# Kernel tuning notes

Hardware: AMD Instinct MI355X
Metric: run time of the kernel (lower is better)

Reference implementation:

```python
import jax, jax.numpy as jnp
import numpy as np
import math

HEAD_DIM = 128
DEPTH = 12
LAMBDA_INIT = 0.8 - 0.6 * math.exp(-0.3 * DEPTH)
EPS = 1e-5


def setup_inputs() -> dict:
    key = jax.random.key(0)
    ks = jax.random.split(key, 7)
    B, S, H2, D = 2, 2048, 16, HEAD_DIM  # H2 = 2 * num_diff_heads
    q = jax.random.normal(ks[0], (B, S, H2, D), dtype=jnp.float32)
    k = jax.random.normal(ks[1], (B, S, H2, D), dtype=jnp.float32)
    v = jax.random.normal(ks[2], (B, S, H2, D), dtype=jnp.float32)
    lambda_q1 = 0.1 * jax.random.normal(ks[3], (D,), dtype=jnp.float32)
    lambda_k1 = 0.1 * jax.random.normal(ks[4], (D,), dtype=jnp.float32)
    lambda_q2 = 0.1 * jax.random.normal(ks[5], (D,), dtype=jnp.float32)
    lambda_k2 = 0.1 * jax.random.normal(ks[6], (D,), dtype=jnp.float32)
    return {"q": q, "k": k, "v": v, "lambda_q1": lambda_q1, "lambda_k1": lambda_k1,
            "lambda_q2": lambda_q2, "lambda_k2": lambda_k2}


def _attn(qh, kh, v12, scale, causal_bias):
    # qh,kh: [B,S,H,D]; v12: [B,S,H,2D] (concat of v1,v2 -> same softmax shared,
    # identical math to the two separate flash calls attnX1/attnX2 concatenated)
    scores = jnp.einsum('bshd,bthd->bhst', qh, kh) * scale + causal_bias
    p = jax.nn.softmax(scores, axis=-1)
    return jnp.einsum('bhst,bthd->bshd', p, v12)  # [B,S,H,2D]


def reference(q, k, v, lambda_q1, lambda_k1, lambda_q2, lambda_k2):
    B, S, H2, D = q.shape
    H = H2 // 2
    scale = 1.0 / math.sqrt(D)
    # split_heads: '(H two) D' -> pairs of adjacent heads
    def split(x):
        x = x.reshape(B, S, H, 2, D)
        return x[..., 0, :], x[..., 1, :]
    q1, q2 = split(q)
    k1, k2 = split(k)
    v1, v2 = split(v)
    v12 = jnp.concatenate([v1, v2], axis=-1)  # [B,S,H,2D]

    causal_bias = jnp.where(jnp.tril(jnp.ones((S, S), dtype=bool)), 0.0,
                            jnp.float32(-jnp.inf))  # [S,S]

    attn1 = _attn(q1, k1, v12, scale, causal_bias)  # = cat(attn11, attn12)
    attn2 = _attn(q2, k2, v12, scale, causal_bias)  # = cat(attn21, attn22)

    lambda_1 = jnp.exp(jnp.sum(lambda_q1 * lambda_k1))
    lambda_2 = jnp.exp(jnp.sum(lambda_q2 * lambda_k2))
    lambda_full = lambda_1 - lambda_2 + LAMBDA_INIT

    attn = attn1 - lambda_full * attn2  # [B,S,H,2D]
    # RMSNorm over last dim (2D), no affine
    attn = attn * jax.lax.rsqrt(jnp.mean(attn * attn, axis=-1, keepdims=True) + EPS)
    attn = attn * (1.0 - LAMBDA_INIT)
    # '... H (two D) -> ... (H two) D'
    return attn.reshape(B, S, H, 2, D).reshape(B, S, H2, D)
```

## Files before the change

kernel.cpp:

```cpp
#include <hip/hip_runtime.h>
#include <math.h>


#define S_LEN 2048
#define ROWSTR 2048
#define NEG_BIG (-3.0e38f)
#define QSCALE (1.44269504088896f * 0.0883883476483184f)
#define LAMBDA_INIT 0.783605766532f

typedef __attribute__((ext_vector_type(8))) short short8;
typedef __attribute__((ext_vector_type(4))) float f32x4;

__device__ __forceinline__ short f2bf(float f) {
    unsigned u = __builtin_bit_cast(unsigned, f);
    u += 0x7fffu + ((u >> 16) & 1u);
    return (short)(u >> 16);
}

__device__ __forceinline__ void async16(const short* g, short* l) {
    __builtin_amdgcn_global_load_lds(
        (const __attribute__((address_space(1))) unsigned int*)g,
        (__attribute__((address_space(3))) unsigned int*)l, 16, 0, 0);
}

__global__ __launch_bounds__(256)
void prep_kernel(const float* __restrict__ q, const float* __restrict__ k,
                 const float* __restrict__ v,
                 short* __restrict__ kws, short* __restrict__ vws,
                 short* __restrict__ qws) {
    const int tid = threadIdx.x;
    const int bh  = blockIdx.x >> 6;
    const int t   = blockIdx.x & 63;
    const int b   = bh >> 3;
    const int h   = bh & 7;

    {
        const int attn = tid >> 7;
        const int key  = (tid >> 2) & 31;
        const int tt   = tid & 3;
        const int s    = t * 32 + key;
        const float* src = k + (((size_t)(b * S_LEN + s) * 16) + 2 * h + attn) * 128 + tt * 32;
        const float* qsrc = q + (((size_t)(b * S_LEN + s) * 16) + 2 * h + attn) * 128 + tt * 32;
        short* kdst = kws + (((size_t)(bh * 64 + t)) << 13) + attn * 4096 + key * 128;
        const int rowtile = s >> 4;
        const int mi      = s & 15;
        short* qdst = qws + (((size_t)(bh * 2 + attn)) << 18) + (rowtile << 11) + (mi << 3);
        #pragma unroll
        for (int i = 0; i < 4; ++i) {
            const int c = tt * 4 + i;
            float4 a0 = *(const float4*)(src + i * 8);
            float4 a1 = *(const float4*)(src + i * 8 + 4);
            short8 sv;
            sv[0]=f2bf(a0.x); sv[1]=f2bf(a0.y); sv[2]=f2bf(a0.z); sv[3]=f2bf(a0.w);
            sv[4]=f2bf(a1.x); sv[5]=f2bf(a1.y); sv[6]=f2bf(a1.z); sv[7]=f2bf(a1.w);
            *(short8*)(kdst + ((c ^ (key & 7)) << 3)) = sv;
            a0 = *(const float4*)(qsrc + i * 8);
            a1 = *(const float4*)(qsrc + i * 8 + 4);
            sv[0]=f2bf(a0.x*QSCALE); sv[1]=f2bf(a0.y*QSCALE); sv[2]=f2bf(a0.z*QSCALE); sv[3]=f2bf(a0.w*QSCALE);
            sv[4]=f2bf(a1.x*QSCALE); sv[5]=f2bf(a1.y*QSCALE); sv[6]=f2bf(a1.z*QSCALE); sv[7]=f2bf(a1.w*QSCALE);
            *(short8*)(qdst + (c << 7)) = sv;
        }
    }

    {
        const int n = tid;
        const float* vsrc = v + (((size_t)(b * S_LEN + t * 32) * 16) + 2 * h + (n >> 7)) * 128 + (n & 127);
        short vv[32];
        #pragma unroll
        for (int key = 0; key < 32; ++key)
            vv[key] = f2bf(vsrc[(size_t)key * ROWSTR]);
        short* vdst = vws + (((size_t)(bh * 64 + t)) << 13) + n * 32;
        #pragma unroll
        for (int i = 0; i < 4; ++i)
            *(short8*)(vdst + i * 8) = *(short8*)&vv[i * 8];
    }
}

__global__ __launch_bounds__(256, 2)
void fda_kernel(const short* __restrict__ kws, const short* __restrict__ vws,
                const short* __restrict__ qws,
                const float* __restrict__ lq1, const float* __restrict__ lk1,
                const float* __restrict__ lq2, const float* __restrict__ lk2,
                float* __restrict__ out) {
    __shared__ short sK[2][2][32][128];
    __shared__ short sV[2][256][32];
    __shared__ short sP[2][64][40];
    __shared__ float sM[2][2];
    __shared__ float sL[2][64];
    __shared__ float sRed[2][2][32];

    const int tid  = threadIdx.x;
    const int w    = tid >> 6;
    const int lane = tid & 63;
    const int mi   = lane & 15;
    const int quad = lane >> 4;
    const int rg   = w & 1;
    const int u    = w >> 1;

    const int bid = blockIdx.x;
    const int bh  = bid & 15;
    const int g   = bid >> 4;
    const int qt  = (g < 16) ? (31 - g) : (g - 16);
    const int b   = bh >> 3;
    const int h   = bh & 7;
    const int qbase = qt * 64;
    const int nt  = 2 * qt + 2;

    float d1 = lq1[lane] * lk1[lane] + lq1[lane + 64] * lk1[lane + 64];
    float d2 = lq2[lane] * lk2[lane] + lq2[lane + 64] * lk2[lane + 64];
    #pragma unroll
    for (int off = 32; off; off >>= 1) {
        d1 += __shfl_xor(d1, off);
        d2 += __shfl_xor(d2, off);
    }
    const float lambda_full = expf(d1) - expf(d2) + LAMBDA_INIT;

    short8 qf[2][4];
    {
        const short* qb = qws + (((size_t)(bh * 2 + u)) << 18);
        #pragma unroll
        for (int m = 0; m < 2; ++m) {
            const int rowtile = qt * 4 + rg * 2 + m;
            #pragma unroll
            for (int db = 0; db < 4; ++db)
                qf[m][db] = *(const short8*)(qb + (rowtile << 11) + (((db << 2) + quad) << 7) + (mi << 3));
        }
    }

    float mold = -1e30f;
    float l[2][4] = {{0.f,0.f,0.f,0.f},{0.f,0.f,0.f,0.f}};
    f32x4 O[2][2][8];
    #pragma unroll
    for (int a = 0; a < 2; ++a)
        #pragma unroll
        for (int m = 0; m < 2; ++m)
            #pragma unroll
            for (int nb = 0; nb < 8; ++nb)
                O[a][m][nb] = (f32x4){0.f, 0.f, 0.f, 0.f};

    const short* ktile0 = kws + (((size_t)(bh * 64)) << 13);
    const short* vtile0 = vws + (((size_t)(bh * 64)) << 13);

    {
        short* dk = &sK[0][0][0][0];
        short* dv = &sV[0][0][0];
        #pragma unroll
        for (int i = 0; i < 4; ++i) {
            const int ch = (w * 4 + i) * 512;
            async16(ktile0 + ch + lane * 8, dk + ch);
            async16(vtile0 + ch + lane * 8, dv + ch);
        }
    }

    for (int t = 0; t < nt; ++t) {
        __syncthreads();
        const int buf = t & 1;
        const bool act = (t <= 2 * qt + rg);

        f32x4 S[2][2];
        if (act) {
            #pragma unroll
            for (int m = 0; m < 2; ++m)
                #pragma unroll
                for (int kh = 0; kh < 2; ++kh)
                    S[m][kh] = (f32x4){0.f, 0.f, 0.f, 0.f};
            const short* kb = &sK[buf][u][0][0];
            #pragma unroll
            for (int db = 0; db < 4; ++db) {
                #pragma unroll
                for (int kh = 0; kh < 2; ++kh) {
                    const short8 kf = *(const short8*)(kb + (kh * 16 + mi) * 128 +
                                       ((((db << 2) + quad) ^ (mi & 7)) << 3));
                    S[0][kh] = __builtin_amdgcn_mfma_f32_16x16x32_bf16(qf[0][db], kf, S[0][kh], 0, 0, 0);
                    S[1][kh] = __builtin_amdgcn_mfma_f32_16x16x32_bf16(qf[1][db], kf, S[1][kh], 0, 0, 0);
                }
            }
            if (t == 2 * qt + rg) {
                const int qr0 = qbase + rg * 32;
                #pragma unroll
                for (int m = 0; m < 2; ++m)
                    #pragma unroll
                    for (int kh = 0; kh < 2; ++kh)
                        #pragma unroll
                        for (int r = 0; r < 4; ++r)
                            if (t * 32 + kh * 16 + mi > qr0 + m * 16 + quad * 4 + r)
                                S[m][kh][r] = NEG_BIG;
            }
            float mx = -1e30f;
            #pragma unroll
            for (int m = 0; m < 2; ++m)
                #pragma unroll
                for (int kh = 0; kh < 2; ++kh)
                    mx = fmaxf(mx, fmaxf(fmaxf(S[m][kh][0], S[m][kh][1]),
                                         fmaxf(S[m][kh][2], S[m][kh][3])));
            #pragma unroll
            for (int off = 32; off; off >>= 1)
                mx = fmaxf(mx, __shfl_xor(mx, off));
            if (lane == 0) sM[rg][u] = mx;
        }
        __syncthreads();

        float alpha = 1.0f;
        if (act) {
            const float mnew = fmaxf(mold, fmaxf(sM[rg][0], sM[rg][1]));
            alpha = exp2f(mold - mnew);
            mold = mnew;
            #pragma unroll
            for (int m = 0; m < 2; ++m) {
                short* pp = &sP[u][rg * 32 + m * 16 + quad * 4][mi];
                #pragma unroll
                for (int r = 0; r < 4; ++r) {
                    const float pa = exp2f(S[m][0][r] - mnew);
                    const float pb = exp2f(S[m][1][r] - mnew);
                    l[m][r] = l[m][r] * alpha + (pa + pb);
                    pp[r * 40]      = f2bf(pa);
                    pp[r * 40 + 16] = f2bf(pb);
                }
            }
        }
        __syncthreads();

        if (t + 1 < nt) {
            const short* kt = ktile0 + (((size_t)(t + 1)) << 13);
            const short* vt = vtile0 + (((size_t)(t + 1)) << 13);
            short* dk = &sK[(t + 1) & 1][0][0][0];
            short* dv = &sV[(t + 1) & 1][0][0];
            #pragma unroll
            for (int i = 0; i < 4; ++i) {
                const int ch = (w * 4 + i) * 512;
                async16(kt + ch + lane * 8, dk + ch);
                async16(vt + ch + lane * 8, dv + ch);
            }
        }

        if (act) {
            if (alpha != 1.0f) {
                #pragma unroll
                for (int a = 0; a < 2; ++a)
                    #pragma unroll
                    for (int m = 0; m < 2; ++m)
                        #pragma unroll
                        for (int nb = 0; nb < 8; ++nb)
                            #pragma unroll
                            for (int r = 0; r < 4; ++r)
                                O[a][m][nb][r] *= alpha;
            }
            short8 pA[2][2];
            #pragma unroll
            for (int a = 0; a < 2; ++a)
                #pragma unroll
                for (int m = 0; m < 2; ++m)
                    pA[a][m] = *(const short8*)&sP[a][rg * 32 + m * 16 + mi][quad * 8];
            #pragma unroll
            for (int nb = 0; nb < 8; ++nb) {
                const short8 bv = *(const short8*)&sV[buf][u * 128 + nb * 16 + mi][quad * 8];
                O[0][0][nb] = __builtin_amdgcn_mfma_f32_16x16x32_bf16(pA[0][0], bv, O[0][0][nb], 0, 0, 0);
                O[0][1][nb] = __builtin_amdgcn_mfma_f32_16x16x32_bf16(pA[0][1], bv, O[0][1][nb], 0, 0, 0);
                O[1][0][nb] = __builtin_amdgcn_mfma_f32_16x16x32_bf16(pA[1][0], bv, O[1][0][nb], 0, 0, 0);
                O[1][1][nb] = __builtin_amdgcn_mfma_f32_16x16x32_bf16(pA[1][1], bv, O[1][1][nb], 0, 0, 0);
            }
        }
    }

    #pragma unroll
    for (int m = 0; m < 2; ++m)
        #pragma unroll
        for (int r = 0; r < 4; ++r) {
            float s = l[m][r];
            s += __shfl_xor(s, 1); s += __shfl_xor(s, 2);
            s += __shfl_xor(s, 4); s += __shfl_xor(s, 8);
            l[m][r] = s;
        }
    if (mi == 0) {
        #pragma unroll
        for (int m = 0; m < 2; ++m)
            #pragma unroll
            for (int r = 0; r < 4; ++r)
                sL[u][rg * 32 + m * 16 + quad * 4 + r] = l[m][r];
    }
    __syncthreads();

    float ss[2][4] = {{0.f,0.f,0.f,0.f},{0.f,0.f,0.f,0.f}};
    #pragma unroll
    for (int m = 0; m < 2; ++m)
        #pragma unroll
        for (int r = 0; r < 4; ++r) {
            const int row = rg * 32 + m * 16 + quad * 4 + r;
            const float il1 = 1.0f / sL[0][row];
            const float il2 = lambda_full / sL[1][row];
            #pragma unroll
            for (int nb = 0; nb < 8; ++nb) {
                const float c = O[0][m][nb][r] * il1 - O[1][m][nb][r] * il2;
                O[0][m][nb][r] = c;
                ss[m][r] += c * c;
            }
        }
    #pragma unroll
    for (int m = 0; m < 2; ++m)
        #pragma unroll
        for (int r = 0; r < 4; ++r) {
            float s = ss[m][r];
            s += __shfl_xor(s, 1); s += __shfl_xor(s, 2);
            s += __shfl_xor(s, 4); s += __shfl_xor(s, 8);
            ss[m][r] = s;
        }
    if (mi == 0) {
        #pragma unroll
        for (int m = 0; m < 2; ++m)
            #pragma unroll
            for (int r = 0; r < 4; ++r)
                sRed[rg][u][m * 16 + quad * 4 + r] = ss[m][r];
    }
    __syncthreads();

    #pragma unroll
    for (int m = 0; m < 2; ++m)
        #pragma unroll
        for (int r = 0; r < 4; ++r) {
            const int rl  = m * 16 + quad * 4 + r;
            const float tot = ss[m][r] + sRed[rg][u ^ 1][rl];
            const float scale = rsqrtf(tot * (1.0f / 256.0f) + 1e-5f) * (1.0f - LAMBDA_INIT);
            const int gr = qbase + rg * 32 + rl;
            float* ob = out + ((size_t)(b * S_LEN + gr)) * ROWSTR + h * 256 + u * 128 + mi;
            #pragma unroll
            for (int nb = 0; nb < 8; ++nb)
                ob[nb * 16] = O[0][m][nb][r] * scale;
        }
}

extern "C" void kernel_launch(void* const* d_in, const int* in_sizes, int n_in,
                              void* d_out, int out_size, void* d_ws, size_t ws_size,
                              hipStream_t stream) {
    (void)in_sizes; (void)n_in; (void)out_size; (void)ws_size;
    const float* q   = (const float*)d_in[0];
    const float* k   = (const float*)d_in[1];
    const float* v   = (const float*)d_in[2];
    const float* lq1 = (const float*)d_in[3];
    const float* lk1 = (const float*)d_in[4];
    const float* lq2 = (const float*)d_in[5];
    const float* lk2 = (const float*)d_in[6];
    float* out = (float*)d_out;

    short* kws = (short*)d_ws;
    short* vws = kws + (size_t)16 * 64 * 8192;
    short* qws = vws + (size_t)16 * 64 * 8192;

    prep_kernel<<<dim3(1024), dim3(256), 0, stream>>>(q, k, v, kws, vws, qws);
    fda_kernel<<<dim3(512), dim3(256), 0, stream>>>(kws, vws, qws,
                                                    lq1, lk1, lq2, lk2, out);
}
```

Baseline: 287.9 us.

## Warp-specialize attention into QK/softmax and PV warps with pipelined tiles

Rewrites the attention kernel to use 512-thread blocks in which four warps compute QK^T and softmax while four other warps compute the PV product one tile behind, passing probabilities and rescale factors through double-buffered shared memory. Each block now processes two query tiles (a long and a short one) to balance causal work, and the grid is halved. Q is converted to bf16 inside the attention kernel instead of in the prep pass, removing the Q workspace round trip. K/V workspace layouts change to remove swizzling, which may introduce LDS bank conflicts, and the larger block may lower occupancy.

Result: slower. 308.4 us (+7.1%).

```diff
diff --git a/kernel.cpp b/kernel.cpp
--- a/kernel.cpp
+++ b/kernel.cpp
@@ -24,10 +24,8 @@
 }
 
 __global__ __launch_bounds__(256)
-void prep_kernel(const float* __restrict__ q, const float* __restrict__ k,
-                 const float* __restrict__ v,
-                 short* __restrict__ kws, short* __restrict__ vws,
-                 short* __restrict__ qws) {
+void prep_kernel(const float* __restrict__ k, const float* __restrict__ v,
+                 short* __restrict__ kws, short* __restrict__ vws) {
     const int tid = threadIdx.x;
     const int bh  = blockIdx.x >> 6;
     const int t   = blockIdx.x & 63;
@@ -37,74 +35,64 @@
     {
         const int attn = tid >> 7;
         const int key  = (tid >> 2) & 31;
-        const int tt   = tid & 3;
-        const int s    = t * 32 + key;
-        const float* src = k + (((size_t)(b * S_LEN + s) * 16) + 2 * h + attn) * 128 + tt * 32;
-        const float* qsrc = q + (((size_t)(b * S_LEN + s) * 16) + 2 * h + attn) * 128 + tt * 32;
-        short* kdst = kws + (((size_t)(bh * 64 + t)) << 13) + attn * 4096 + key * 128;
-        const int rowtile = s >> 4;
-        const int mi      = s & 15;
-        short* qdst = qws + (((size_t)(bh * 2 + attn)) << 18) + (rowtile << 11) + (mi << 3);
+        const int dg   = tid & 3;
+        const float* src = k + ((size_t)(b * S_LEN + t * 32 + key) * 16 + 2 * h + attn) * 128 + dg * 32;
+        short* dstb = kws + ((size_t)(bh * 64 + t) << 13) + attn * 4096 + key * 8;
         #pragma unroll
         for (int i = 0; i < 4; ++i) {
-            const int c = tt * 4 + i;
-            float4 a0 = *(const float4*)(src + i * 8);
-            float4 a1 = *(const float4*)(src + i * 8 + 4);
+            const float4 a0 = *(const float4*)(src + i * 8);
+            const float4 a1 = *(const float4*)(src + i * 8 + 4);
             short8 sv;
             sv[0]=f2bf(a0.x); sv[1]=f2bf(a0.y); sv[2]=f2bf(a0.z); sv[3]=f2bf(a0.w);
             sv[4]=f2bf(a1.x); sv[5]=f2bf(a1.y); sv[6]=f2bf(a1.z); sv[7]=f2bf(a1.w);
-            *(short8*)(kdst + ((c ^ (key & 7)) << 3)) = sv;
-            a0 = *(const float4*)(qsrc + i * 8);
-            a1 = *(const float4*)(qsrc + i * 8 + 4);
-            sv[0]=f2bf(a0.x*QSCALE); sv[1]=f2bf(a0.y*QSCALE); sv[2]=f2bf(a0.z*QSCALE); sv[3]=f2bf(a0.w*QSCALE);
-            sv[4]=f2bf(a1.x*QSCALE); sv[5]=f2bf(a1.y*QSCALE); sv[6]=f2bf(a1.z*QSCALE); sv[7]=f2bf(a1.w*QSCALE);
-            *(short8*)(qdst + (c << 7)) = sv;
+            *(short8*)(dstb + (dg * 4 + i) * 256) = sv;
         }
     }
-
     {
         const int n = tid;
-        const float* vsrc = v + (((size_t)(b * S_LEN + t * 32) * 16) + 2 * h + (n >> 7)) * 128 + (n & 127);
+        const float* vsrc = v + ((size_t)(b * S_LEN + t * 32) * 16 + 2 * h + (n >> 7)) * 128 + (n & 127);
         short vv[32];
         #pragma unroll
         for (int key = 0; key < 32; ++key)
             vv[key] = f2bf(vsrc[(size_t)key * ROWSTR]);
-        short* vdst = vws + (((size_t)(bh * 64 + t)) << 13) + n * 32;
+        short* vdst = vws + ((size_t)(bh * 64 + t) << 13) + n * 8;
         #pragma unroll
-        for (int i = 0; i < 4; ++i)
-            *(short8*)(vdst + i * 8) = *(short8*)&vv[i * 8];
+        for (int kc = 0; kc < 4; ++kc)
+            *(short8*)(vdst + kc * 2048) = *(short8*)&vv[kc * 8];
     }
 }
 
-__global__ __launch_bounds__(256, 2)
+__global__ __launch_bounds__(512, 2)
 void fda_kernel(const short* __restrict__ kws, const short* __restrict__ vws,
-                const short* __restrict__ qws,
+                const float* __restrict__ q,
                 const float* __restrict__ lq1, const float* __restrict__ lk1,
                 const float* __restrict__ lq2, const float* __restrict__ lk2,
                 float* __restrict__ out) {
-    __shared__ short sK[2][2][32][128];
-    __shared__ short sV[2][256][32];
-    __shared__ short sP[2][64][40];
-    __shared__ float sM[2][2];
+    __shared__ short sK[2][8192];
+    __shared__ short sV[2][8192];
+    __shared__ short sP[2][2][64][40];
+    __shared__ float sAl[2][2][2];
     __shared__ float sL[2][64];
-    __shared__ float sRed[2][2][32];
+    __shared__ float sRed[4][64];
 
     const int tid  = threadIdx.x;
     const int w    = tid >> 6;
     const int lane = tid & 63;
     const int mi   = lane & 15;
     const int quad = lane >> 4;
-    const int rg   = w & 1;
-    const int u    = w >> 1;
-
-    const int bid = blockIdx.x;
-    const int bh  = bid & 15;
-    const int g   = bid >> 4;
-    const int qt  = (g < 16) ? (31 - g) : (g - 16);
-    const int b   = bh >> 3;
-    const int h   = bh & 7;
-    const int qbase = qt * 64;
-    const int nt  = 2 * qt + 2;
+
+    const int bh = blockIdx.x & 15;
+    const int g  = blockIdx.x >> 4;
+    const int b  = bh >> 3;
+    const int h  = bh & 7;
+
+    const bool isQK = (w < 4);
+    const int u  = w & 1;
+    const int mh = (w >> 1) & 1;
+    const int nq = w - 4;
+
+    const short* ktile0 = kws + ((size_t)(bh * 64) << 13);
+    const short* vtile0 = vws + ((size_t)(bh * 64) << 13);
 
     float d1 = lq1[lane] * lk1[lane] + lq1[lane + 64] * lk1[lane + 64];
     float d2 = lq2[lane] * lk2[lane] + lq2[lane + 64] * lk2[lane + 64];
@@ -115,217 +103,254 @@
     }
     const float lambda_full = expf(d1) - expf(d2) + LAMBDA_INIT;
 
-    short8 qf[2][4];
-    {
-        const short* qb = qws + (((size_t)(bh * 2 + u)) << 18);
-        #pragma unroll
-        for (int m = 0; m < 2; ++m) {
-            const int rowtile = qt * 4 + rg * 2 + m;
-            #pragma unroll
-            for (int db = 0; db < 4; ++db)
-                qf[m][db] = *(const short8*)(qb + (rowtile << 11) + (((db << 2) + quad) << 7) + (mi << 3));
-        }
-    }
-
-    float mold = -1e30f;
-    float l[2][4] = {{0.f,0.f,0.f,0.f},{0.f,0.f,0.f,0.f}};
-    f32x4 O[2][2][8];
-    #pragma unroll
-    for (int a = 0; a < 2; ++a)
-        #pragma unroll
-        for (int m = 0; m < 2; ++m)
-            #pragma unroll
-            for (int nb = 0; nb < 8; ++nb)
-                O[a][m][nb] = (f32x4){0.f, 0.f, 0.f, 0.f};
-
-    const short* ktile0 = kws + (((size_t)(bh * 64)) << 13);
-    const short* vtile0 = vws + (((size_t)(bh * 64)) << 13);
-
-    {
-        short* dk = &sK[0][0][0][0];
-        short* dv = &sV[0][0][0];
-        #pragma unroll
-        for (int i = 0; i < 4; ++i) {
-            const int ch = (w * 4 + i) * 512;
-            async16(ktile0 + ch + lane * 8, dk + ch);
-            async16(vtile0 + ch + lane * 8, dv + ch);
-        }
-    }
-
-    for (int t = 0; t < nt; ++t) {
+    for (int ph = 0; ph < 2; ++ph) {
+        const int qt = ph ? g : (31 - g);
+        const int qbase = qt * 64;
+        const int nt = 2 * qt + 2;
+
+        short8 qf[2][4];
+        float mold = -1e30f;
+        float lsum[2][4] = {{0.f,0.f,0.f,0.f},{0.f,0.f,0.f,0.f}};
+        f32x4 O[2][4][4];
+
+        if (isQK) {
+            const short* src = ktile0 + u * 4096 + mh * 2048 + lane * 8;
+            short* dst = &sK[0][u * 4096 + mh * 2048 + lane * 8];
+            #pragma unroll
+            for (int c = 0; c < 4; ++c) async16(src + c * 512, dst + c * 512);
+            #pragma unroll
+            for (int m = 0; m < 2; ++m) {
+                const float* p0 = q + ((size_t)(b * S_LEN + qbase + mh * 32 + m * 16 + mi) * 16 + 2 * h + u) * 128 + quad * 8;
+                #pragma unroll
+                for (int db = 0; db < 4; ++db) {
+                    const float* p = p0 + db * 32;
+                    const float4 a0 = *(const float4*)p;
+                    const float4 a1 = *(const float4*)(p + 4);
+                    short8 f;
+                    f[0]=f2bf(a0.x*QSCALE); f[1]=f2bf(a0.y*QSCALE);
+                    f[2]=f2bf(a0.z*QSCALE); f[3]=f2bf(a0.w*QSCALE);
+                    f[4]=f2bf(a1.x*QSCALE); f[5]=f2bf(a1.y*QSCALE);
+                    f[6]=f2bf(a1.z*QSCALE); f[7]=f2bf(a1.w*QSCALE);
+                    qf[m][db] = f;
+                }
+            }
+        } else {
+            const short* src = vtile0 + nq * 512 + lane * 8;
+            short* dst = &sV[0][nq * 512 + lane * 8];
+            #pragma unroll
+            for (int kc = 0; kc < 4; ++kc) async16(src + kc * 2048, dst + kc * 2048);
+            #pragma unroll
+            for (int a = 0; a < 2; ++a)
+                #pragma unroll
+                for (int m = 0; m < 4; ++m)
+                    #pragma unroll
+                    for (int nb = 0; nb < 4; ++nb)
+                        O[a][m][nb] = (f32x4){0.f, 0.f, 0.f, 0.f};
+        }
         __syncthreads();
-        const int buf = t & 1;
-        const bool act = (t <= 2 * qt + rg);
-
-        f32x4 S[2][2];
-        if (act) {
-            #pragma unroll
-            for (int m = 0; m < 2; ++m)
-                #pragma unroll
-                for (int kh = 0; kh < 2; ++kh)
-                    S[m][kh] = (f32x4){0.f, 0.f, 0.f, 0.f};
-            const short* kb = &sK[buf][u][0][0];
-            #pragma unroll
-            for (int db = 0; db < 4; ++db) {
-                #pragma unroll
-                for (int kh = 0; kh < 2; ++kh) {
-                    const short8 kf = *(const short8*)(kb + (kh * 16 + mi) * 128 +
-                                       ((((db << 2) + quad) ^ (mi & 7)) << 3));
-                    S[0][kh] = __builtin_amdgcn_mfma_f32_16x16x32_bf16(qf[0][db], kf, S[0][kh], 0, 0, 0);
-                    S[1][kh] = __builtin_amdgcn_mfma_f32_16x16x32_bf16(qf[1][db], kf, S[1][kh], 0, 0, 0);
-                }
-            }
-            if (t == 2 * qt + rg) {
-                const int qr0 = qbase + rg * 32;
+
+        for (int t = 0; t < nt; ++t) {
+            const int buf = t & 1;
+            if (isQK) {
+                f32x4 S[2][2];
                 #pragma unroll
                 for (int m = 0; m < 2; ++m)
                     #pragma unroll
                     for (int kh = 0; kh < 2; ++kh)
-                        #pragma unroll
-                        for (int r = 0; r < 4; ++r)
-                            if (t * 32 + kh * 16 + mi > qr0 + m * 16 + quad * 4 + r)
-                                S[m][kh][r] = NEG_BIG;
-            }
-            float mx = -1e30f;
-            #pragma unroll
-            for (int m = 0; m < 2; ++m)
-                #pragma unroll
-                for (int kh = 0; kh < 2; ++kh)
-                    mx = fmaxf(mx, fmaxf(fmaxf(S[m][kh][0], S[m][kh][1]),
-                                         fmaxf(S[m][kh][2], S[m][kh][3])));
-            #pragma unroll
-            for (int off = 32; off; off >>= 1)
-                mx = fmaxf(mx, __shfl_xor(mx, off));
-            if (lane == 0) sM[rg][u] = mx;
-        }
-        __syncthreads();
-
-        float alpha = 1.0f;
-        if (act) {
-            const float mnew = fmaxf(mold, fmaxf(sM[rg][0], sM[rg][1]));
-            alpha = exp2f(mold - mnew);
-            mold = mnew;
-            #pragma unroll
-            for (int m = 0; m < 2; ++m) {
-                short* pp = &sP[u][rg * 32 + m * 16 + quad * 4][mi];
-                #pragma unroll
-                for (int r = 0; r < 4; ++r) {
-                    const float pa = exp2f(S[m][0][r] - mnew);
-                    const float pb = exp2f(S[m][1][r] - mnew);
-                    l[m][r] = l[m][r] * alpha + (pa + pb);
-                    pp[r * 40]      = f2bf(pa);
-                    pp[r * 40 + 16] = f2bf(pb);
-                }
-            }
-        }
-        __syncthreads();
-
-        if (t + 1 < nt) {
-            const short* kt = ktile0 + (((size_t)(t + 1)) << 13);
-            const short* vt = vtile0 + (((size_t)(t + 1)) << 13);
-            short* dk = &sK[(t + 1) & 1][0][0][0];
-            short* dv = &sV[(t + 1) & 1][0][0];
-            #pragma unroll
-            for (int i = 0; i < 4; ++i) {
-                const int ch = (w * 4 + i) * 512;
-                async16(kt + ch + lane * 8, dk + ch);
-                async16(vt + ch + lane * 8, dv + ch);
-            }
-        }
-
-        if (act) {
-            if (alpha != 1.0f) {
-                #pragma unroll
-                for (int a = 0; a < 2; ++a)
+                        S[m][kh] = (f32x4){0.f, 0.f, 0.f, 0.f};
+                const short* kb = &sK[buf][u * 4096];
+                #pragma unroll
+                for (int db = 0; db < 4; ++db) {
+                    #pragma unroll
+                    for (int kh = 0; kh < 2; ++kh) {
+                        const short8 kf = *(const short8*)(kb + (db * 4 + quad) * 256 + (kh * 16 + mi) * 8);
+                        S[0][kh] = __builtin_amdgcn_mfma_f32_16x16x32_bf16(qf[0][db], kf, S[0][kh], 0, 0, 0);
+                        S[1][kh] = __builtin_amdgcn_mfma_f32_16x16x32_bf16(qf[1][db], kf, S[1][kh], 0, 0, 0);
+                    }
+                }
+                if (t + 1 < nt) {
+                    const short* src = ktile0 + ((size_t)(t + 1) << 13) + u * 4096 + mh * 2048 + lane * 8;
+                    short* dst = &sK[buf ^ 1][u * 4096 + mh * 2048 + lane * 8];
+                    #pragma unroll
+                    for (int c = 0; c < 4; ++c) async16(src + c * 512, dst + c * 512);
+                }
+                if (t >= 2 * qt + mh) {
+                    const int r0 = qbase + mh * 32;
                     #pragma unroll
                     for (int m = 0; m < 2; ++m)
                         #pragma unroll
-                        for (int nb = 0; nb < 8; ++nb)
+                        for (int kh = 0; kh < 2; ++kh)
                             #pragma unroll
                             for (int r = 0; r < 4; ++r)
-                                O[a][m][nb][r] *= alpha;
+                                if (t * 32 + kh * 16 + mi > r0 + m * 16 + quad * 4 + r)
+                                    S[m][kh][r] = NEG_BIG;
+                }
+                float mx = NEG_BIG;
+                #pragma unroll
+                for (int m = 0; m < 2; ++m)
+                    #pragma unroll
+                    for (int kh = 0; kh < 2; ++kh)
+                        mx = fmaxf(mx, fmaxf(fmaxf(S[m][kh][0], S[m][kh][1]),
+                                             fmaxf(S[m][kh][2], S[m][kh][3])));
+                #pragma unroll
+                for (int off = 32; off; off >>= 1)
+                    mx = fmaxf(mx, __shfl_xor(mx, off));
+                const float mnew = fmaxf(mold, mx);
+                const float alpha = exp2f(mold - mnew);
+                mold = mnew;
+                #pragma unroll
+                for (int m = 0; m < 2; ++m) {
+                    short* pp = &sP[buf][u][mh * 32 + m * 16 + quad * 4][mi];
+                    #pragma unroll
+                    for (int r = 0; r < 4; ++r) {
+                        const float pa = exp2f(S[m][0][r] - mnew);
+                        const float pb = exp2f(S[m][1][r] - mnew);
+                        lsum[m][r] = lsum[m][r] * alpha + (pa + pb);
+                        pp[r * 40]      = f2bf(pa);
+                        pp[r * 40 + 16] = f2bf(pb);
+                    }
+                }
+                if (lane == 0) sAl[buf][u][mh] = alpha;
+            } else {
+                if (t > 0) {
+                    const int pbuf = (t - 1) & 1;
+                    const float a00 = sAl[pbuf][0][0], a01 = sAl[pbuf][0][1];
+                    const float a10 = sAl[pbuf][1][0], a11 = sAl[pbuf][1][1];
+                    if (a00 != 1.f || a01 != 1.f || a10 != 1.f || a11 != 1.f) {
+                        #pragma unroll
+                        for (int m = 0; m < 4; ++m) {
+                            const float aa0 = (m < 2) ? a00 : a01;
+                            const float aa1 = (m < 2) ? a10 : a11;
+                            #pragma unroll
+                            for (int nb = 0; nb < 4; ++nb)
+                                #pragma unroll
+                                for (int r = 0; r < 4; ++r) {
+                                    O[0][m][nb][r] *= aa0;
+                                    O[1][m][nb][r] *= aa1;
+                                }
+                        }
+                    }
+                    short8 pA[2][4];
+                    #pragma unroll
+                    for (int a = 0; a < 2; ++a)
+                        #pragma unroll
+                        for (int m = 0; m < 4; ++m)
+                            pA[a][m] = *(const short8*)&sP[pbuf][a][m * 16 + mi][quad * 8];
+                    short8 bv[4];
+                    #pragma unroll
+                    for (int nb = 0; nb < 4; ++nb)
+                        bv[nb] = *(const short8*)&sV[pbuf][quad * 2048 + (nq * 64 + nb * 16 + mi) * 8];
+                    #pragma unroll
+                    for (int nb = 0; nb < 4; ++nb)
+                        #pragma unroll
+                        for (int a = 0; a < 2; ++a)
+                            #pragma unroll
+                            for (int m = 0; m < 4; ++m)
+                                O[a][m][nb] = __builtin_amdgcn_mfma_f32_16x16x32_bf16(pA[a][m], bv[nb], O[a][m][nb], 0, 0, 0);
+                    if (t + 1 < nt) {
+                        const short* src = vtile0 + ((size_t)(t + 1) << 13) + nq * 512 + lane * 8;
+                        short* dst = &sV[buf ^ 1][nq * 512 + lane * 8];
+                        #pragma unroll
+                        for (int kc = 0; kc < 4; ++kc) async16(src + kc * 2048, dst + kc * 2048);
+                    }
+                } else {
+                    const short* src = vtile0 + ((size_t)1 << 13) + nq * 512 + lane * 8;
+                    short* dst = &sV[1][nq * 512 + lane * 8];
+                    #pragma unroll
+                    for (int kc = 0; kc < 4; ++kc) async16(src + kc * 2048, dst + kc * 2048);
+                }
             }
-            short8 pA[2][2];
+            __syncthreads();
+        }
+
+        if (isQK) {
+            #pragma unroll
+            for (int m = 0; m < 2; ++m)
+                #pragma unroll
+                for (int r = 0; r < 4; ++r) {
+                    float s = lsum[m][r];
+                    s += __shfl_xor(s, 1); s += __shfl_xor(s, 2);
+                    s += __shfl_xor(s, 4); s += __shfl_xor(s, 8);
+                    if (mi == 0) sL[u][mh * 32 + m * 16 + quad * 4 + r] = s;
+                }
+        } else {
+            const int pbuf = (nt - 1) & 1;
+            const float a00 = sAl[pbuf][0][0], a01 = sAl[pbuf][0][1];
+            const float a10 = sAl[pbuf][1][0], a11 = sAl[pbuf][1][1];
+            if (a00 != 1.f || a01 != 1.f || a10 != 1.f || a11 != 1.f) {
+                #pragma unroll
+                for (int m = 0; m < 4; ++m) {
+                    const float aa0 = (m < 2) ? a00 : a01;
+                    const float aa1 = (m < 2) ? a10 : a11;
+                    #pragma unroll
+                    for (int nb = 0; nb < 4; ++nb)
+                        #pragma unroll
+                        for (int r = 0; r < 4; ++r) {
+                            O[0][m][nb][r] *= aa0;
+                            O[1][m][nb][r] *= aa1;
+                        }
+                }
+            }
+            short8 pA[2][4];
             #pragma unroll
             for (int a = 0; a < 2; ++a)
                 #pragma unroll
-                for (int m = 0; m < 2; ++m)
-                    pA[a][m] = *(const short8*)&sP[a][rg * 32 + m * 16 + mi][quad * 8];
-            #pragma unroll
-            for (int nb = 0; nb < 8; ++nb) {
-                const short8 bv = *(const short8*)&sV[buf][u * 128 + nb * 16 + mi][quad * 8];
-                O[0][0][nb] = __builtin_amdgcn_mfma_f32_16x16x32_bf16(pA[0][0], bv, O[0][0][nb], 0, 0, 0);
-                O[0][1][nb] = __builtin_amdgcn_mfma_f32_16x16x32_bf16(pA[0][1], bv, O[0][1][nb], 0, 0, 0);
-                O[1][0][nb] = __builtin_amdgcn_mfma_f32_16x16x32_bf16(pA[1][0], bv, O[1][0][nb], 0, 0, 0);
-                O[1][1][nb] = __builtin_amdgcn_mfma_f32_16x16x32_bf16(pA[1][1], bv, O[1][1][nb], 0, 0, 0);
-            }
-        }
+                for (int m = 0; m < 4; ++m)
+                    pA[a][m] = *(const short8*)&sP[pbuf][a][m * 16 + mi][quad * 8];
+            short8 bv[4];
+            #pragma unroll
+            for (int nb = 0; nb < 4; ++nb)
+                bv[nb] = *(const short8*)&sV[pbuf][quad * 2048 + (nq * 64 + nb * 16 + mi) * 8];
+            #pragma unroll
+            for (int nb = 0; nb < 4; ++nb)
+                #pragma unroll
+                for (int a = 0; a < 2; ++a)
+                    #pragma unroll
+                    for (int m = 0; m < 4; ++m)
+                        O[a][m][nb] = __builtin_amdgcn_mfma_f32_16x16x32_bf16(pA[a][m], bv[nb], O[a][m][nb], 0, 0, 0);
+        }
+        __syncthreads();
+
+        float ss[4][4];
+        if (!isQK) {
+            #pragma unroll
+            for (int m = 0; m < 4; ++m)
+                #pragma unroll
+                for (int r = 0; r < 4; ++r) {
+                    const int row = m * 16 + quad * 4 + r;
+                    const float il1 = 1.0f / sL[0][row];
+                    const float il2 = lambda_full / sL[1][row];
+                    float acc = 0.f;
+                    #pragma unroll
+                    for (int nb = 0; nb < 4; ++nb) {
+                        const float c = O[0][m][nb][r] * il1 - O[1][m][nb][r] * il2;
+                        O[0][m][nb][r] = c;
+                        acc += c * c;
+                    }
+                    acc += __shfl_xor(acc, 1); acc += __shfl_xor(acc, 2);
+                    acc += __shfl_xor(acc, 4); acc += __shfl_xor(acc, 8);
+                    ss[m][r] = acc;
+                    if (mi == 0) sRed[nq][row] = acc;
+                }
+        }
+        __syncthreads();
+
+        if (!isQK) {
+            #pragma unroll
+            for (int m = 0; m < 4; ++m)
+                #pragma unroll
+                for (int r = 0; r < 4; ++r) {
+                    const int row = m * 16 + quad * 4 + r;
+                    const float tot = sRed[0][row] + sRed[1][row] + sRed[2][row] + sRed[3][row];
+                    const float scale = rsqrtf(tot * (1.0f / 256.0f) + 1e-5f) * (1.0f - LAMBDA_INIT);
+                    float* ob = out + ((size_t)(b * S_LEN + qbase + row)) * ROWSTR + h * 256 + nq * 64 + mi;
+                    #pragma unroll
+                    for (int nb = 0; nb < 4; ++nb)
+                        ob[nb * 16] = O[0][m][nb][r] * scale;
+                }
+        }
+        __syncthreads();
     }
-
-    #pragma unroll
-    for (int m = 0; m < 2; ++m)
-        #pragma unroll
-        for (int r = 0; r < 4; ++r) {
-            float s = l[m][r];
-            s += __shfl_xor(s, 1); s += __shfl_xor(s, 2);
-            s += __shfl_xor(s, 4); s += __shfl_xor(s, 8);
-            l[m][r] = s;
-        }
-    if (mi == 0) {
-        #pragma unroll
-        for (int m = 0; m < 2; ++m)
-            #pragma unroll
-            for (int r = 0; r < 4; ++r)
-                sL[u][rg * 32 + m * 16 + quad * 4 + r] = l[m][r];
-    }
-    __syncthreads();
-
-    float ss[2][4] = {{0.f,0.f,0.f,0.f},{0.f,0.f,0.f,0.f}};
-    #pragma unroll
-    for (int m = 0; m < 2; ++m)
-        #pragma unroll
-        for (int r = 0; r < 4; ++r) {
-            const int row = rg * 32 + m * 16 + quad * 4 + r;
-            const float il1 = 1.0f / sL[0][row];
-            const float il2 = lambda_full / sL[1][row];
-            #pragma unroll
-            for (int nb = 0; nb < 8; ++nb) {
-                const float c = O[0][m][nb][r] * il1 - O[1][m][nb][r] * il2;
-                O[0][m][nb][r] = c;
-                ss[m][r] += c * c;
-            }
-        }
-    #pragma unroll
-    for (int m = 0; m < 2; ++m)
-        #pragma unroll
-        for (int r = 0; r < 4; ++r) {
-            float s = ss[m][r];
-            s += __shfl_xor(s, 1); s += __shfl_xor(s, 2);
-            s += __shfl_xor(s, 4); s += __shfl_xor(s, 8);
-            ss[m][r] = s;
-        }
-    if (mi == 0) {
-        #pragma unroll
-        for (int m = 0; m < 2; ++m)
-            #pragma unroll
-            for (int r = 0; r < 4; ++r)
-                sRed[rg][u][m * 16 + quad * 4 + r] = ss[m][r];
-    }
-    __syncthreads();
-
-    #pragma unroll
-    for (int m = 0; m < 2; ++m)
-        #pragma unroll
-        for (int r = 0; r < 4; ++r) {
-            const int rl  = m * 16 + quad * 4 + r;
-            const float tot = ss[m][r] + sRed[rg][u ^ 1][rl];
-            const float scale = rsqrtf(tot * (1.0f / 256.0f) + 1e-5f) * (1.0f - LAMBDA_INIT);
-            const int gr = qbase + rg * 32 + rl;
-            float* ob = out + ((size_t)(b * S_LEN + gr)) * ROWSTR + h * 256 + u * 128 + mi;
-            #pragma unroll
-            for (int nb = 0; nb < 8; ++nb)
-                ob[nb * 16] = O[0][m][nb][r] * scale;
-        }
 }
 
 extern "C" void kernel_launch(void* const* d_in, const int* in_sizes, int n_in,
@@ -343,9 +368,8 @@
 
     short* kws = (short*)d_ws;
     short* vws = kws + (size_t)16 * 64 * 8192;
-    short* qws = vws + (size_t)16 * 64 * 8192;
-
-    prep_kernel<<<dim3(1024), dim3(256), 0, stream>>>(q, k, v, kws, vws, qws);
-    fda_kernel<<<dim3(512), dim3(256), 0, stream>>>(kws, vws, qws,
+
+    prep_kernel<<<dim3(1024), dim3(256), 0, stream>>>(k, v, kws, vws);
+    fda_kernel<<<dim3(256), dim3(512), 0, stream>>>(kws, vws, q,
                                                     lq1, lk1, lq2, lk2, out);
 }
```
